# Performance work log

Measured on AMD Instinct MI355X. Metric: run time of the kernel, lower is better.

The kernel has to match this reference:

```python
import math
import jax, jax.numpy as jnp
import numpy as np

W_BITS = 8
A_BITS = 8
N_HEADS = 16

def fake_quant(x, bits):
    # symmetric per-tensor fake quantization with straight-through estimator
    if bits >= 32:
        return x
    qmax = float(2 ** (bits - 1) - 1)
    scale = jnp.maximum(jnp.max(jnp.abs(x)) / qmax, 1e-8)
    q = jnp.round(x / scale) * scale
    return x + jax.lax.stop_gradient(q - x)

def qlinear(x, W, b):
    # QuantizeLinear: quantize activations (a_bits) and weights (w_bits), then y = x @ W^T + b
    xq = fake_quant(x, A_BITS)
    Wq = fake_quant(W, W_BITS)
    return jnp.einsum('bsd,ed->bse', xq, Wq) + b

def setup_inputs() -> dict:
    key = jax.random.key(0)
    B, S, D = 2, 2048, 1024
    ks = jax.random.split(key, 6)
    inp = {
        'hidden_states': jax.random.normal(ks[0], (B, S, D), dtype=jnp.float32),
        'attention_mask': jnp.ones((B, S), dtype=jnp.float32),
        'Wq': 0.02 * jax.random.normal(ks[1], (D, D), dtype=jnp.float32),
        'bq': jnp.zeros((D,), dtype=jnp.float32),
        'Wk': 0.02 * jax.random.normal(ks[2], (D, D), dtype=jnp.float32),
        'bk': jnp.zeros((D,), dtype=jnp.float32),
        'Wv': 0.02 * jax.random.normal(ks[3], (D, D), dtype=jnp.float32),
        'bv': jnp.zeros((D,), dtype=jnp.float32),
        'Wo': 0.02 * jax.random.normal(ks[4], (D, D), dtype=jnp.float32),
        'bo': jnp.zeros((D,), dtype=jnp.float32),
    }
    return inp

def reference(hidden_states, attention_mask, Wq, bq, Wk, bk, Wv, bv, Wo, bo):
    B, S, D = hidden_states.shape
    H = N_HEADS
    hd = D // H

    q = qlinear(hidden_states, Wq, bq).reshape(B, S, H, hd)
    k = qlinear(hidden_states, Wk, bk).reshape(B, S, H, hd)
    v = qlinear(hidden_states, Wv, bv).reshape(B, S, H, hd)

    # scores: [B, H, Sq, Sk]
    scores = jnp.einsum('bqhd,bkhd->bhqk', q, k) / math.sqrt(hd)
    mask_bias = (1.0 - attention_mask)[:, None, None, :] * -10000.0
    scores = scores + mask_bias
    probs = jax.nn.softmax(scores, axis=-1)

    attn = jnp.einsum('bhqk,bkhd->bqhd', probs, v).reshape(B, S, D)
    return qlinear(attn, Wo, bo)
```

## Files before the change

kernel.cpp:

```cpp
#include <hip/hip_runtime.h>
#include <cstddef>
#include <cstdint>

constexpr int Bb = 2, Ss = 2048, Dd = 1024, Hh = 16, HD = 64;
constexpr int Mm = Bb * Ss;

typedef int v4i __attribute__((ext_vector_type(4)));
typedef __bf16 bf16x8 __attribute__((ext_vector_type(8)));
typedef __bf16 bf16x2 __attribute__((ext_vector_type(2)));
typedef float f32x16 __attribute__((ext_vector_type(16)));

#define QPOSTMUL 0.18033688f
#define MASKBIAS -14426.950408f

__device__ __forceinline__ float qscale(float amax) {
    return fmaxf(amax / 127.0f, 1e-8f);
}

__device__ __forceinline__ unsigned short bf16rtn(float x) {
    __bf16 b = (__bf16)x;
    return __builtin_bit_cast(unsigned short, b);
}

__device__ __forceinline__ unsigned pack_bf16x2(float a, float b) {
    unsigned ua = __float_as_uint(a), ub = __float_as_uint(b);
    unsigned ha = (ua + 0x7fffu + ((ua >> 16) & 1u)) >> 16;
    unsigned hb = (ub + 0x7fffu + ((ub >> 16) & 1u)) & 0xffff0000u;
    return ha | hb;
}

__global__ void amax_all(const float4* __restrict__ hidden,
                         const float4* __restrict__ w0, const float4* __restrict__ w1,
                         const float4* __restrict__ w2, const float4* __restrict__ w3,
                         unsigned* __restrict__ slots) {
    const float4* src; int n4, slot, bx, nb;
    if (blockIdx.x < 448) { src = hidden; n4 = Mm * Dd / 4; slot = 0; bx = blockIdx.x; nb = 448; }
    else {
        int w = (blockIdx.x - 448) >> 4; bx = (blockIdx.x - 448) & 15; nb = 16;
        src = w == 0 ? w0 : w == 1 ? w1 : w == 2 ? w2 : w3;
        n4 = Dd * Dd / 4; slot = 1 + w;
    }
    float m = 0.f;
    for (int i = bx * blockDim.x + threadIdx.x; i < n4; i += nb * blockDim.x) {
        float4 v = src[i];
        m = fmaxf(m, fmaxf(fmaxf(fabsf(v.x), fabsf(v.y)), fmaxf(fabsf(v.z), fabsf(v.w))));
    }
    #pragma unroll
    for (int off = 32; off > 0; off >>= 1) m = fmaxf(m, __shfl_down(m, off, 64));
    __shared__ float sm[4];
    int lane = threadIdx.x & 63, wid = threadIdx.x >> 6;
    if (lane == 0) sm[wid] = m;
    __syncthreads();
    if (threadIdx.x == 0) {
        float mm = fmaxf(fmaxf(sm[0], sm[1]), fmaxf(sm[2], sm[3]));
        atomicMax(slots + slot, __float_as_uint(mm));
    }
}

__global__ void quant_all(const float* __restrict__ hidden,
                          const float* __restrict__ w0, const float* __restrict__ w1,
                          const float* __restrict__ w2, const float* __restrict__ w3,
                          const float* __restrict__ amax,
                          char* __restrict__ hq8, char* __restrict__ Wall8) {
    const float* x; char* y; int n4, slot, bx, nb;
    if (blockIdx.x < 1024) { x = hidden; y = hq8; n4 = Mm * Dd / 4; slot = 0; bx = blockIdx.x; nb = 1024; }
    else {
        int w = (blockIdx.x - 1024) >> 5; bx = (blockIdx.x - 1024) & 31; nb = 32;
        x = w == 0 ? w0 : w == 1 ? w1 : w == 2 ? w2 : w3;
        y = Wall8 + ((size_t)w << 20);
        n4 = Dd * Dd / 4; slot = 1 + w;
    }
    float s = qscale(amax[slot]);
    const float4* x4 = (const float4*)x;
    char4* y4 = (char4*)y;
    for (int i = bx * blockDim.x + threadIdx.x; i < n4; i += nb * blockDim.x) {
        float4 v = x4[i];
        char4 q;
        q.x = (char)(int)rintf(v.x / s);
        q.y = (char)(int)rintf(v.y / s);
        q.z = (char)(int)rintf(v.z / s);
        q.w = (char)(int)rintf(v.w / s);
        y4[i] = q;
    }
}

__global__ void quant_a(const float* __restrict__ x, char* __restrict__ y,
                        const float* __restrict__ amax, int n4) {
    float s = qscale(amax[0]);
    int stride = gridDim.x * blockDim.x;
    const float4* x4 = (const float4*)x;
    char4* y4 = (char4*)y;
    for (int i = blockIdx.x * blockDim.x + threadIdx.x; i < n4; i += stride) {
        float4 v = x4[i];
        char4 q;
        q.x = (char)(int)rintf(v.x / s);
        q.y = (char)(int)rintf(v.y / s);
        q.z = (char)(int)rintf(v.z / s);
        q.w = (char)(int)rintf(v.w / s);
        y4[i] = q;
    }
}

#define GLOAD_LDS16(g, l) __builtin_amdgcn_global_load_lds( \
    (const __attribute__((address_space(1))) unsigned int*)(g), \
    (__attribute__((address_space(3))) unsigned int*)(l), 16, 0, 0)

__device__ __forceinline__ void gemm128_core(const char* __restrict__ A, const char* __restrict__ Bw,
                                             int bm, int bn, int K, int t,
                                             char* At, char* Bt, v4i acc[4][4]) {
    const int lane = t & 63, w = t >> 6;
    const int wm = (w >> 1) * 64, wn = (w & 1) * 64;
    const int lr = lane & 15, kq = lane >> 4;
    const int rs = w * 16 + (lane >> 2);
    const int cc = lane & 3;

    for (int k0 = 0; k0 < K; k0 += 64) {
        __syncthreads();
        #pragma unroll
        for (int h = 0; h < 2; h++) {
            int r = rs + h * 64;
            int cs = cc ^ ((r >> 1) & 3);
            GLOAD_LDS16(A  + (size_t)(bm + r) * K + k0 + cs * 16, At + r * 64 + cc * 16);
            GLOAD_LDS16(Bw + (size_t)(bn + r) * K + k0 + cs * 16, Bt + r * 64 + cc * 16);
        }
        __syncthreads();

        v4i af[4], bf[4];
        #pragma unroll
        for (int mt = 0; mt < 4; mt++) {
            int row = wm + mt * 16 + lr;
            af[mt] = *(const v4i*)(At + row * 64 + ((kq ^ ((row >> 1) & 3)) << 4));
        }
        #pragma unroll
        for (int nt = 0; nt < 4; nt++) {
            int row = wn + nt * 16 + lr;
            bf[nt] = *(const v4i*)(Bt + row * 64 + ((kq ^ ((row >> 1) & 3)) << 4));
        }
        #pragma unroll
        for (int mt = 0; mt < 4; mt++)
            #pragma unroll
            for (int nt = 0; nt < 4; nt++)
                acc[mt][nt] = __builtin_amdgcn_mfma_i32_16x16x64_i8(af[mt], bf[nt], acc[mt][nt], 0, 0, 0);
    }
}

__global__ __launch_bounds__(256) void gemm_qkv(const char* __restrict__ A,
                                                const char* __restrict__ Wall8,
                                                const float* __restrict__ bq,
                                                const float* __restrict__ bk,
                                                const float* __restrict__ bv,
                                                const float* __restrict__ amax,
                                                unsigned short* __restrict__ qb16,
                                                unsigned short* __restrict__ kb16,
                                                unsigned short* __restrict__ vt16) {
    __shared__ alignas(16) char pool[34816];
    char* At = pool;
    char* Bt = pool + 8192;
    unsigned short (*Tt)[136] = (unsigned short(*)[136])pool;

    const int t = threadIdx.x, lane = t & 63, w = t >> 6;
    const int mat = blockIdx.x >> 3;
    const int bn = (blockIdx.x & 7) * 128, bm = blockIdx.y * 128;
    const int wm = (w >> 1) * 64, wn = (w & 1) * 64;
    const int lr = lane & 15, kq = lane >> 4;

    const v4i vzero = {0, 0, 0, 0};
    v4i acc[4][4];
    #pragma unroll
    for (int mt = 0; mt < 4; mt++)
        #pragma unroll
        for (int nt = 0; nt < 4; nt++) acc[mt][nt] = vzero;

    const char* Bw = Wall8 + ((size_t)mat << 20);
    gemm128_core(A, Bw, bm, bn, Dd, t, At, Bt, acc);

    const float* bias = mat == 0 ? bq : mat == 1 ? bk : bv;
    float sc = qscale(amax[0]) * qscale(amax[1 + mat]);
    float pm = (mat == 0) ? QPOSTMUL : 1.0f;

    __syncthreads();

    if (mat != 2) {
        #pragma unroll
        for (int nt = 0; nt < 4; nt++) {
            int n_l = wn + nt * 16 + lr;
            float bv_ = bias[bn + n_l];
            #pragma unroll
            for (int mt = 0; mt < 4; mt++) {
                int m_l = wm + mt * 16 + kq * 4;
                #pragma unroll
                for (int rg = 0; rg < 4; rg++)
                    Tt[m_l + rg][n_l] = bf16rtn(((float)acc[mt][nt][rg] * sc + bv_) * pm);
            }
        }
    } else {
        #pragma unroll
        for (int nt = 0; nt < 4; nt++) {
            int n_l = wn + nt * 16 + lr;
            float bv_ = bias[bn + n_l];
            #pragma unroll
            for (int mt = 0; mt < 4; mt++) {
                int m_l = wm + mt * 16 + kq * 4;
                ushort4 hv;
                hv.x = bf16rtn((float)acc[mt][nt][0] * sc + bv_);
                hv.y = bf16rtn((float)acc[mt][nt][1] * sc + bv_);
                hv.z = bf16rtn((float)acc[mt][nt][2] * sc + bv_);
                hv.w = bf16rtn((float)acc[mt][nt][3] * sc + bv_);
                *(ushort4*)&Tt[n_l][m_l] = hv;
            }
        }
    }
    __syncthreads();

    {
        int row = t >> 1, half = t & 1;
        unsigned short* dst;
        if (mat != 2) {
            dst = (mat == 0 ? qb16 : kb16) + (size_t)(bm + row) * Dd + bn + half * 64;
        } else {
            int n = bn + row;
            int e = n & 63, hc = n >> 6;
            int b_ = bm >> 11, s_ = (bm & 2047) + half * 64;
            dst = vt16 + (((size_t)(b_ * Hh + hc) * 64 + e) * Ss) + s_;
        }
        const unsigned short* srcl = &Tt[row][half * 64];
        #pragma unroll
        for (int c = 0; c < 8; c++)
            *(int4*)(dst + c * 8) = *(const int4*)(srcl + c * 8);
    }
}

__global__ __launch_bounds__(256) void gemm_o(const char* __restrict__ A,
                                              const char* __restrict__ Bw,
                                              const float* __restrict__ bias,
                                              const float* __restrict__ amaxA,
                                              const float* __restrict__ amaxB,
                                              float* __restrict__ C) {
    __shared__ alignas(16) char At[128 * 64];
    __shared__ alignas(16) char Bt[64 * 64];
    const int t = threadIdx.x, lane = t & 63, w = t >> 6;
    const int bn = blockIdx.x * 64, bm = blockIdx.y * 128;
    const int wm = (w >> 1) * 64, wn = (w & 1) * 32;
    const int lr = lane & 15, kq = lane >> 4;
    const int rs = t >> 2, cc = t & 3;
    const int cs = cc ^ ((rs >> 1) & 3);
    const int rs2 = rs + 64, cs2 = cc ^ ((rs2 >> 1) & 3);

    const v4i vzero = {0, 0, 0, 0};
    v4i acc[4][2];
    #pragma unroll
    for (int mt = 0; mt < 4; mt++) { acc[mt][0] = vzero; acc[mt][1] = vzero; }

    for (int k0 = 0; k0 < Dd; k0 += 64) {
        __syncthreads();
        GLOAD_LDS16(A  + (size_t)(bm + rs)  * Dd + k0 + cs  * 16, At + rs  * 64 + cc * 16);
        GLOAD_LDS16(A  + (size_t)(bm + rs2) * Dd + k0 + cs2 * 16, At + rs2 * 64 + cc * 16);
        GLOAD_LDS16(Bw + (size_t)(bn + rs)  * Dd + k0 + cs  * 16, Bt + rs  * 64 + cc * 16);
        __syncthreads();

        v4i af[4], bf[2];
        #pragma unroll
        for (int mt = 0; mt < 4; mt++) {
            int row = wm + mt * 16 + lr;
            af[mt] = *(const v4i*)(At + row * 64 + ((kq ^ ((row >> 1) & 3)) << 4));
        }
        #pragma unroll
        for (int nt = 0; nt < 2; nt++) {
            int row = wn + nt * 16 + lr;
            bf[nt] = *(const v4i*)(Bt + row * 64 + ((kq ^ ((row >> 1) & 3)) << 4));
        }
        #pragma unroll
        for (int mt = 0; mt < 4; mt++)
            #pragma unroll
            for (int nt = 0; nt < 2; nt++)
                acc[mt][nt] = __builtin_amdgcn_mfma_i32_16x16x64_i8(af[mt], bf[nt], acc[mt][nt], 0, 0, 0);
    }

    float sc = qscale(amaxA[0]) * qscale(amaxB[0]);
    #pragma unroll
    for (int nt = 0; nt < 2; nt++) {
        int n = bn + wn + nt * 16 + lr;
        float bv_ = bias[n];
        #pragma unroll
        for (int mt = 0; mt < 4; mt++)
            #pragma unroll
            for (int rg = 0; rg < 4; rg++) {
                int m = bm + wm + mt * 16 + kq * 4 + rg;
                C[(size_t)m * Dd + n] = (float)acc[mt][nt][rg] * sc + bv_;
            }
    }
}

__global__ __launch_bounds__(256) void attn_mfma(
    const unsigned short* __restrict__ qb16, const unsigned short* __restrict__ kb16,
    const unsigned short* __restrict__ vt16,
    const float* __restrict__ mask, float* __restrict__ Ob, unsigned* __restrict__ amax_out) {
    __shared__ alignas(16) unsigned short KsHi[64][72], VsHi[64][72];
    __shared__ alignas(16) unsigned PwU[4][32][36];
    __shared__ float mbias[64];
    __shared__ float wred[4];

    const int t = threadIdx.x, lane = t & 63, wq = t >> 6;
    const int ln31 = lane & 31, h5 = lane >> 5;
    const int b = blockIdx.z, h = blockIdx.y, q0 = blockIdx.x * 128;

    bf16x8 qf[4];
    {
        int qrow = q0 + wq * 32 + ln31;
        const unsigned short* qb_ = qb16 + ((size_t)(b * Ss + qrow)) * Dd + h * 64 + h5 * 8;
        #pragma unroll
        for (int c = 0; c < 4; c++) qf[c] = *(const bf16x8*)(qb_ + c * 16);
    }

    const int srow = t >> 2, cp = (t & 3) * 2;
    const int rho = (srow >> 1) + (srow & 1) * 32;
    int4 pk0, pk1, pv0, pv1; float pmask = 1.f;
    auto prefetch = [&](int k0) {
        const unsigned short* gk = kb16 + ((size_t)(b * Ss + k0 + srow)) * Dd + h * 64 + cp * 8;
        const unsigned short* gv = vt16 + (((size_t)(b * Hh + h) * 64 + srow)) * Ss + k0 + cp * 8;
        pk0 = *(const int4*)gk; pk1 = *(const int4*)(gk + 8);
        pv0 = *(const int4*)gv; pv1 = *(const int4*)(gv + 8);
        if (t < 64) pmask = mask[b * Ss + k0 + t];
    };

    f32x16 o0 = 0.f, o1 = 0.f;
    float lp[16];
    #pragma unroll
    for (int r = 0; r < 16; r++) lp[r] = 0.f;

    prefetch(0);
    for (int k0 = 0; k0 < Ss; k0 += 64) {
        __syncthreads();
        *(int4*)&KsHi[rho][cp * 8]      = pk0;
        *(int4*)&KsHi[rho][cp * 8 + 8]  = pk1;
        *(int4*)&VsHi[srow][cp * 8]     = pv0;
        *(int4*)&VsHi[srow][cp * 8 + 8] = pv1;
        if (t < 64) mbias[t] = (1.0f - pmask) * MASKBIAS;
        __syncthreads();
        if (k0 + 64 < Ss) prefetch(k0 + 64);

        f32x16 sc0 = 0.f, sc1 = 0.f;
        #pragma unroll
        for (int c = 0; c < 4; c++) {
            bf16x8 kh0 = *(const bf16x8*)&KsHi[ln31][c * 16 + h5 * 8];
            bf16x8 kh1 = *(const bf16x8*)&KsHi[32 + ln31][c * 16 + h5 * 8];
            sc0 = __builtin_amdgcn_mfma_f32_32x32x16_bf16(qf[c], kh0, sc0, 0, 0, 0);
            sc1 = __builtin_amdgcn_mfma_f32_32x32x16_bf16(qf[c], kh1, sc1, 0, 0, 0);
        }

        float mb0 = mbias[2 * ln31], mb1 = mbias[2 * ln31 + 1];
        #pragma unroll
        for (int r = 0; r < 16; r++) {
            float p0 = __builtin_amdgcn_exp2f(sc0[r] + mb0);
            float p1 = __builtin_amdgcn_exp2f(sc1[r] + mb1);
            lp[r] += p0 + p1;
            int row = (r & 3) + 8 * (r >> 2) + 4 * h5;
            PwU[wq][row][ln31] = pack_bf16x2(p0, p1);
        }

        #pragma unroll
        for (int c = 0; c < 4; c++) {
            bf16x8 pf = *(const bf16x8*)((const unsigned short*)&PwU[wq][ln31][0] + c * 16 + h5 * 8);
            bf16x8 vh0 = *(const bf16x8*)&VsHi[ln31][c * 16 + h5 * 8];
            bf16x8 vh1 = *(const bf16x8*)&VsHi[32 + ln31][c * 16 + h5 * 8];
            o0 = __builtin_amdgcn_mfma_f32_32x32x16_bf16(pf, vh0, o0, 0, 0, 0);
            o1 = __builtin_amdgcn_mfma_f32_32x32x16_bf16(pf, vh1, o1, 0, 0, 0);
        }
    }

    float lmax = 0.f;
    #pragma unroll
    for (int r = 0; r < 16; r++) {
        float l = lp[r];
        #pragma unroll
        for (int off = 1; off < 32; off <<= 1) l += __shfl_xor(l, off, 32);
        float inv = 1.0f / l;
        int row = q0 + wq * 32 + (r & 3) + 8 * (r >> 2) + 4 * h5;
        size_t ro = ((size_t)(b * Ss + row)) * Dd + h * 64;
        float v0 = o0[r] * inv, v1 = o1[r] * inv;
        Ob[ro + ln31] = v0;
        Ob[ro + 32 + ln31] = v1;
        lmax = fmaxf(lmax, fmaxf(fabsf(v0), fabsf(v1)));
    }
    #pragma unroll
    for (int off = 32; off > 0; off >>= 1) lmax = fmaxf(lmax, __shfl_xor(lmax, off, 64));
    if (lane == 0) wred[wq] = lmax;
    __syncthreads();
    if (t == 0) {
        float m = fmaxf(fmaxf(wred[0], wred[1]), fmaxf(wred[2], wred[3]));
        atomicMax(amax_out, __float_as_uint(m));
    }
}

extern "C" void kernel_launch(void* const* d_in, const int* in_sizes, int n_in,
                              void* d_out, int out_size, void* d_ws, size_t ws_size,
                              hipStream_t stream) {
    const float* hidden = (const float*)d_in[0];
    const float* mask   = (const float*)d_in[1];
    const float* Wq = (const float*)d_in[2];
    const float* bq = (const float*)d_in[3];
    const float* Wk = (const float*)d_in[4];
    const float* bk = (const float*)d_in[5];
    const float* Wv = (const float*)d_in[6];
    const float* bv = (const float*)d_in[7];
    const float* Wo = (const float*)d_in[8];
    const float* bo = (const float*)d_in[9];
    float* out = (float*)d_out;

    char* ws = (char*)d_ws;
    float* scal = (float*)ws;
    size_t off = 1024;
    const size_t szH8 = (size_t)Mm * Dd;
    const size_t szHb = (size_t)Mm * Dd * sizeof(unsigned short);
    const size_t szHf = (size_t)Mm * Dd * sizeof(float);
    char* hq8   = ws + off; off += szH8;
    char* Wall8 = ws + off; off += 4u << 20;
    char* aq8   = ws + off; off += szH8;
    unsigned short* qb16 = (unsigned short*)(ws + off); off += szHb;
    unsigned short* kb16 = (unsigned short*)(ws + off); off += szHb;
    unsigned short* vt16 = (unsigned short*)(ws + off); off += szHb;
    float* ab = (float*)(ws + off); off += szHf;

    hipMemsetAsync(scal, 0, 64, stream);

    amax_all<<<512, 256, 0, stream>>>((const float4*)hidden, (const float4*)Wq,
                                      (const float4*)Wk, (const float4*)Wv, (const float4*)Wo,
                                      (unsigned*)scal);
    quant_all<<<1152, 256, 0, stream>>>(hidden, Wq, Wk, Wv, Wo, scal, hq8, Wall8);

    gemm_qkv<<<dim3(24, 32), 256, 0, stream>>>(hq8, Wall8, bq, bk, bv, scal,
                                               qb16, kb16, vt16);

    attn_mfma<<<dim3(Ss / 128, Hh, Bb), 256, 0, stream>>>(qb16, kb16, vt16,
                                                          mask, ab, (unsigned*)(scal + 5));

    quant_a<<<1024, 256, 0, stream>>>(ab, aq8, scal + 5, Mm * Dd / 4);

    gemm_o<<<dim3(16, 32), 256, 0, stream>>>(aq8, Wall8 + (3u << 20), bo,
                                             scal + 5, scal + 4, out);
}
```

Before: 230.6 us.

## Transpose attention MFMA operands to keep probabilities in registers

The QK^T and PV MFMAs now take K and V as the A operand and Q and P as the B operand. Each lane then holds a query column of scores, so the softmax row sum reduces to one scalar per lane and the probabilities reach the PV MFMA through a cross-half lane shuffle instead of a per-iteration LDS round trip. A block-wide ballot skips the mask-bias add when every key in the tile is unmasked. Output is staged through reused shared memory so global stores become coalesced float4 writes. The cost is extra shuffles and selects in the inner loop, plus a shared-memory flag read per tile.

After: 230.7 us. About the same (+0.0%).

```diff
diff --git a/kernel.cpp b/kernel.cpp
--- a/kernel.cpp
+++ b/kernel.cpp
@@ -7,7 +7,6 @@
 
 typedef int v4i __attribute__((ext_vector_type(4)));
 typedef __bf16 bf16x8 __attribute__((ext_vector_type(8)));
-typedef __bf16 bf16x2 __attribute__((ext_vector_type(2)));
 typedef float f32x16 __attribute__((ext_vector_type(16)));
 
 #define QPOSTMUL 0.18033688f
@@ -295,92 +294,125 @@
     const unsigned short* __restrict__ qb16, const unsigned short* __restrict__ kb16,
     const unsigned short* __restrict__ vt16,
     const float* __restrict__ mask, float* __restrict__ Ob, unsigned* __restrict__ amax_out) {
-    __shared__ alignas(16) unsigned short KsHi[64][72], VsHi[64][72];
-    __shared__ alignas(16) unsigned PwU[4][32][36];
-    __shared__ float mbias[64];
+    __shared__ alignas(16) char pool[18688];
+    unsigned short (*Ks)[72] = (unsigned short(*)[72])pool;
+    unsigned short (*Vs)[72] = (unsigned short(*)[72])(pool + 9216);
+    float* mbias = (float*)(pool + 18432);
+    __shared__ int mflag;
     __shared__ float wred[4];
 
     const int t = threadIdx.x, lane = t & 63, wq = t >> 6;
     const int ln31 = lane & 31, h5 = lane >> 5;
-    const int b = blockIdx.z, h = blockIdx.y, q0 = blockIdx.x * 128;
+    const int b = blockIdx.z, head = blockIdx.y, q0 = blockIdx.x * 128;
 
     bf16x8 qf[4];
     {
         int qrow = q0 + wq * 32 + ln31;
-        const unsigned short* qb_ = qb16 + ((size_t)(b * Ss + qrow)) * Dd + h * 64 + h5 * 8;
+        const unsigned short* qb_ = qb16 + ((size_t)(b * Ss + qrow)) * Dd + head * 64 + h5 * 8;
         #pragma unroll
         for (int c = 0; c < 4; c++) qf[c] = *(const bf16x8*)(qb_ + c * 16);
     }
 
     const int srow = t >> 2, cp = (t & 3) * 2;
-    const int rho = (srow >> 1) + (srow & 1) * 32;
     int4 pk0, pk1, pv0, pv1; float pmask = 1.f;
     auto prefetch = [&](int k0) {
-        const unsigned short* gk = kb16 + ((size_t)(b * Ss + k0 + srow)) * Dd + h * 64 + cp * 8;
-        const unsigned short* gv = vt16 + (((size_t)(b * Hh + h) * 64 + srow)) * Ss + k0 + cp * 8;
+        const unsigned short* gk = kb16 + ((size_t)(b * Ss + k0 + srow)) * Dd + head * 64 + cp * 8;
+        const unsigned short* gv = vt16 + (((size_t)(b * Hh + head) * 64 + srow)) * Ss + k0 + cp * 8;
         pk0 = *(const int4*)gk; pk1 = *(const int4*)(gk + 8);
         pv0 = *(const int4*)gv; pv1 = *(const int4*)(gv + 8);
         if (t < 64) pmask = mask[b * Ss + k0 + t];
     };
 
     f32x16 o0 = 0.f, o1 = 0.f;
-    float lp[16];
-    #pragma unroll
-    for (int r = 0; r < 16; r++) lp[r] = 0.f;
+    float lp = 0.f;
 
     prefetch(0);
     for (int k0 = 0; k0 < Ss; k0 += 64) {
         __syncthreads();
-        *(int4*)&KsHi[rho][cp * 8]      = pk0;
-        *(int4*)&KsHi[rho][cp * 8 + 8]  = pk1;
-        *(int4*)&VsHi[srow][cp * 8]     = pv0;
-        *(int4*)&VsHi[srow][cp * 8 + 8] = pv1;
-        if (t < 64) mbias[t] = (1.0f - pmask) * MASKBIAS;
+        *(int4*)&Ks[srow][cp * 8]     = pk0;
+        *(int4*)&Ks[srow][cp * 8 + 8] = pk1;
+        *(int4*)&Vs[srow][cp * 8]     = pv0;
+        *(int4*)&Vs[srow][cp * 8 + 8] = pv1;
+        if (t < 64) {
+            mbias[t] = (1.0f - pmask) * MASKBIAS;
+            unsigned long long bal = __ballot(pmask == 1.0f);
+            if (t == 0) mflag = (bal == ~0ull) ? 1 : 0;
+        }
         __syncthreads();
         if (k0 + 64 < Ss) prefetch(k0 + 64);
 
         f32x16 sc0 = 0.f, sc1 = 0.f;
         #pragma unroll
         for (int c = 0; c < 4; c++) {
-            bf16x8 kh0 = *(const bf16x8*)&KsHi[ln31][c * 16 + h5 * 8];
-            bf16x8 kh1 = *(const bf16x8*)&KsHi[32 + ln31][c * 16 + h5 * 8];
-            sc0 = __builtin_amdgcn_mfma_f32_32x32x16_bf16(qf[c], kh0, sc0, 0, 0, 0);
-            sc1 = __builtin_amdgcn_mfma_f32_32x32x16_bf16(qf[c], kh1, sc1, 0, 0, 0);
-        }
-
-        float mb0 = mbias[2 * ln31], mb1 = mbias[2 * ln31 + 1];
+            bf16x8 ka = *(const bf16x8*)&Ks[ln31][c * 16 + h5 * 8];
+            bf16x8 kb = *(const bf16x8*)&Ks[32 + ln31][c * 16 + h5 * 8];
+            sc0 = __builtin_amdgcn_mfma_f32_32x32x16_bf16(ka, qf[c], sc0, 0, 0, 0);
+            sc1 = __builtin_amdgcn_mfma_f32_32x32x16_bf16(kb, qf[c], sc1, 0, 0, 0);
+        }
+
+        unsigned pp0[8], pp1[8];
+        const bool allone = (mflag != 0);
+        #pragma unroll
+        for (int i = 0; i < 8; i++) {
+            float a0, a1, b0, b1;
+            if (allone) {
+                a0 = sc0[2 * i]; a1 = sc0[2 * i + 1];
+                b0 = sc1[2 * i]; b1 = sc1[2 * i + 1];
+            } else {
+                int r = 2 * i;
+                int ky0 = (r & 3) + 8 * (r >> 2) + 4 * h5;
+                int ky1 = ((r + 1) & 3) + 8 * ((r + 1) >> 2) + 4 * h5;
+                a0 = sc0[r] + mbias[ky0];     a1 = sc0[r + 1] + mbias[ky1];
+                b0 = sc1[r] + mbias[32 + ky0]; b1 = sc1[r + 1] + mbias[32 + ky1];
+            }
+            float e00 = __builtin_amdgcn_exp2f(a0), e01 = __builtin_amdgcn_exp2f(a1);
+            float e10 = __builtin_amdgcn_exp2f(b0), e11 = __builtin_amdgcn_exp2f(b1);
+            lp += (e00 + e01) + (e10 + e11);
+            pp0[i] = pack_bf16x2(e00, e01);
+            pp1[i] = pack_bf16x2(e10, e11);
+        }
+
+        #pragma unroll
+        for (int c = 0; c < 4; c++) {
+            const unsigned* pp = (c < 2) ? pp0 : pp1;
+            const int cb = (c & 1) * 4;
+            unsigned a0 = pp[cb], a1 = pp[cb + 1], b0 = pp[cb + 2], b1 = pp[cb + 3];
+            unsigned own0 = h5 ? b0 : a0, own1 = h5 ? b1 : a1;
+            unsigned snd0 = h5 ? a0 : b0, snd1 = h5 ? a1 : b1;
+            unsigned rc0 = (unsigned)__shfl_xor((int)snd0, 32, 64);
+            unsigned rc1 = (unsigned)__shfl_xor((int)snd1, 32, 64);
+            union { unsigned u[4]; bf16x8 v; } pf;
+            pf.u[0] = h5 ? rc0 : own0;
+            pf.u[1] = h5 ? rc1 : own1;
+            pf.u[2] = h5 ? own0 : rc0;
+            pf.u[3] = h5 ? own1 : rc1;
+            bf16x8 av0 = *(const bf16x8*)&Vs[ln31][c * 16 + h5 * 8];
+            bf16x8 av1 = *(const bf16x8*)&Vs[32 + ln31][c * 16 + h5 * 8];
+            o0 = __builtin_amdgcn_mfma_f32_32x32x16_bf16(av0, pf.v, o0, 0, 0, 0);
+            o1 = __builtin_amdgcn_mfma_f32_32x32x16_bf16(av1, pf.v, o1, 0, 0, 0);
+        }
+    }
+
+    float inv = 1.0f / (lp + __shfl_xor(lp, 32, 64));
+    __syncthreads();
+    float (*Otr)[36] = (float(*)[36])(pool + wq * 4608);
+    float lmax = 0.f;
+    #pragma unroll
+    for (int rh = 0; rh < 2; rh++) {
+        const f32x16& oh = rh ? o1 : o0;
         #pragma unroll
         for (int r = 0; r < 16; r++) {
-            float p0 = __builtin_amdgcn_exp2f(sc0[r] + mb0);
-            float p1 = __builtin_amdgcn_exp2f(sc1[r] + mb1);
-            lp[r] += p0 + p1;
-            int row = (r & 3) + 8 * (r >> 2) + 4 * h5;
-            PwU[wq][row][ln31] = pack_bf16x2(p0, p1);
-        }
-
+            int e = (r & 3) + 8 * (r >> 2) + 4 * h5;
+            Otr[ln31][e] = oh[r] * inv;
+        }
         #pragma unroll
         for (int c = 0; c < 4; c++) {
-            bf16x8 pf = *(const bf16x8*)((const unsigned short*)&PwU[wq][ln31][0] + c * 16 + h5 * 8);
-            bf16x8 vh0 = *(const bf16x8*)&VsHi[ln31][c * 16 + h5 * 8];
-            bf16x8 vh1 = *(const bf16x8*)&VsHi[32 + ln31][c * 16 + h5 * 8];
-            o0 = __builtin_amdgcn_mfma_f32_32x32x16_bf16(pf, vh0, o0, 0, 0, 0);
-            o1 = __builtin_amdgcn_mfma_f32_32x32x16_bf16(pf, vh1, o1, 0, 0, 0);
-        }
-    }
-
-    float lmax = 0.f;
-    #pragma unroll
-    for (int r = 0; r < 16; r++) {
-        float l = lp[r];
-        #pragma unroll
-        for (int off = 1; off < 32; off <<= 1) l += __shfl_xor(l, off, 32);
-        float inv = 1.0f / l;
-        int row = q0 + wq * 32 + (r & 3) + 8 * (r >> 2) + 4 * h5;
-        size_t ro = ((size_t)(b * Ss + row)) * Dd + h * 64;
-        float v0 = o0[r] * inv, v1 = o1[r] * inv;
-        Ob[ro + ln31] = v0;
-        Ob[ro + 32 + ln31] = v1;
-        lmax = fmaxf(lmax, fmaxf(fabsf(v0), fabsf(v1)));
+            int row = (lane >> 3) + 8 * c;
+            float4 v = *(const float4*)&Otr[row][(lane & 7) * 4];
+            lmax = fmaxf(lmax, fmaxf(fmaxf(fabsf(v.x), fabsf(v.y)), fmaxf(fabsf(v.z), fabsf(v.w))));
+            size_t ro = ((size_t)(b * Ss + q0 + wq * 32 + row)) * Dd + head * 64 + rh * 32 + (lane & 7) * 4;
+            *(float4*)&Ob[ro] = v;
+        }
     }
     #pragma unroll
     for (int off = 32; off > 0; off >>= 1) lmax = fmaxf(lmax, __shfl_xor(lmax, off, 64));
```
